# Optimization experiments

Hardware: AMD Instinct MI355X
Metric: run time of the kernel (lower is better)

The kernel has to match this reference:

```python
import jax, jax.numpy as jnp
import numpy as np

BN_EPS = 1e-5


def setup_inputs() -> dict:
    key = jax.random.key(0)
    ks = jax.random.split(key, 12)
    N, F, H, E, ED, G, EMB = 59392, 116, 256, 950272, 5, 8, 16
    return {
        "x": jax.random.normal(ks[0], (N, F), dtype=jnp.float32),
        "edge_index": jax.random.randint(ks[1], (2, E), 0, N, dtype=jnp.int64),
        "edge_attr": jax.random.normal(ks[2], (E, ED), dtype=jnp.float32),
        "group_ids": jax.random.randint(ks[3], (N,), 0, G, dtype=jnp.int64),
        "group_emb": jax.random.normal(ks[4], (G, EMB), dtype=jnp.float32),
        "W_in": jax.random.normal(ks[5], (F + EMB, H), dtype=jnp.float32) * 0.05,
        "b_in": jnp.zeros((H,), dtype=jnp.float32),
        "gamma": jnp.ones((H,), dtype=jnp.float32),
        "beta": jnp.zeros((H,), dtype=jnp.float32),
        "We": jax.random.normal(ks[6], (ED, H), dtype=jnp.float32) * 0.05,
        "be": jnp.zeros((H,), dtype=jnp.float32),
        "W1": jax.random.normal(ks[7], (H, H), dtype=jnp.float32) * 0.05,
        "b1": jnp.zeros((H,), dtype=jnp.float32),
        "W2": jax.random.normal(ks[8], (H, H), dtype=jnp.float32) * 0.05,
        "b2": jnp.zeros((H,), dtype=jnp.float32),
    }


def reference(x, edge_index, edge_attr, group_ids, group_emb, W_in, b_in,
              gamma, beta, We, be, W1, b1, W2, b2):
    N = x.shape[0]
    # group-embedding concat (dropout is identity in eval mode)
    h = jnp.concatenate([x, group_emb[group_ids]], axis=-1)      # [N, F+EMB]
    # dynamically-created Linear + ReLU
    h = jax.nn.relu(h @ W_in + b_in)                              # [N, H]
    # BatchNorm over nodes (training stats, biased var)
    mu = jnp.mean(h, axis=0)
    var = jnp.mean(jnp.square(h - mu), axis=0)
    h = (h - mu) * jax.lax.rsqrt(var + BN_EPS) * gamma + beta
    # GINEConv: msg = ReLU(x_j + lin(edge_attr)); sum-aggregate at target
    src, dst = edge_index[0], edge_index[1]
    msg = jax.nn.relu(h[src] + edge_attr @ We + be)               # [E, H]
    agg = jax.ops.segment_sum(msg, dst, num_segments=N)          # [N, H]
    z = h + agg                                                   # (1+eps)*h, eps=0
    out = jax.nn.relu(z @ W1 + b1) @ W2 + b2                      # 2-layer MLP
    out = jax.nn.relu(out)
    return (out, edge_attr)
```

## Files before the change

### kernel.cpp

```cpp
#include <hip/hip_runtime.h>
#include <hip/hip_bf16.h>
#include <cstdint>
#include <cstddef>

#define H 256
#define EMB 16
#define ED 5
#define BN_EPS 1e-5f

typedef __attribute__((ext_vector_type(8))) short short8;
typedef __attribute__((ext_vector_type(4))) float f32x4;
typedef _Float16 h2 __attribute__((ext_vector_type(2)));
typedef unsigned int u32x2 __attribute__((ext_vector_type(2)));

__device__ __forceinline__ unsigned short f2bf(float f) {
  unsigned int u = __float_as_uint(f);
  unsigned int r = (u + 0x7fffu + ((u >> 16) & 1u)) >> 16;
  return (unsigned short)r;
}
__device__ __forceinline__ unsigned int pk2bf(float a, float b) {
  return (unsigned int)f2bf(a) | ((unsigned int)f2bf(b) << 16);
}
__device__ __forceinline__ float bfhi(unsigned int u) {
  return __uint_as_float(u & 0xffff0000u);
}
__device__ __forceinline__ float bflo(unsigned int u) {
  return __uint_as_float(u << 16);
}
__device__ __forceinline__ h2 u2h2(unsigned int u) {
  union { unsigned int u; h2 h; } c;
  c.u = u;
  return c.h;
}
__device__ __forceinline__ unsigned int h22u(h2 h) {
  union { h2 h; unsigned int u; } c;
  c.h = h;
  return c.u;
}
__device__ __forceinline__ h2 mkh2(float a, float b) {
  h2 r;
  r.x = (_Float16)a;
  r.y = (_Float16)b;
  return r;
}

__global__ __launch_bounds__(256) void prep_kernel(
    const float* __restrict__ Win, const float* __restrict__ W1,
    const float* __restrict__ W2, const float* __restrict__ gemb,
    const float* __restrict__ b_in, unsigned short* __restrict__ Wtx,
    unsigned short* __restrict__ Wt1, unsigned short* __restrict__ Wt2,
    float* __restrict__ T, float* __restrict__ stats, int* __restrict__ deg,
    unsigned short* __restrict__ hbn, uint4* __restrict__ rec,
    int N, int F, int G, int E) {
  int idx = blockIdx.x * 256 + threadIdx.x;
  if (idx < 1024) stats[idx] = 0.f;
  if (idx < N) deg[idx] = 0;
  if (idx < 32)
    ((uint4*)(hbn + (size_t)N * H))[idx] =
        make_uint4(0xF400F400u, 0xF400F400u, 0xF400F400u, 0xF400F400u);
  if (idx == 0) rec[E] = make_uint4(((unsigned)N) << 9, 0u, 0u, 0u);
  if (idx < 256 * 128) {
    int n = idx >> 7, k = idx & 127;
    Wtx[idx] = f2bf((k < F) ? Win[(size_t)k * H + n] : 0.f);
  } else if (idx < 256 * 128 + 65536) {
    int i2 = idx - 256 * 128;
    int n = i2 >> 8, k = i2 & 255;
    Wt1[i2] = f2bf(W1[(size_t)k * H + n]);
  } else if (idx < 256 * 128 + 131072) {
    int i2 = idx - 256 * 128 - 65536;
    int n = i2 >> 8, k = i2 & 255;
    Wt2[i2] = f2bf(W2[(size_t)k * H + n]);
  } else if (idx < 256 * 128 + 131072 + G * 256) {
    int i2 = idx - 256 * 128 - 131072;
    int g = i2 >> 8, c = i2 & 255;
    float s = b_in[c];
    #pragma unroll
    for (int k = 0; k < EMB; ++k)
      s = fmaf(gemb[g * EMB + k], Win[(size_t)(F + k) * H + c], s);
    T[i2] = s;
  }
}

__global__ __launch_bounds__(256) void gemm_in_kernel(
    const float* __restrict__ x, const int* __restrict__ gid,
    const unsigned short* __restrict__ Wtx, const float* __restrict__ T,
    unsigned short* __restrict__ h0, float* __restrict__ stats, int F) {
  const int m0 = blockIdx.y * 128;
  const int n0 = blockIdx.x * 128;
  const int tid = threadIdx.x;
  const int lane = tid & 63;
  const int wave = tid >> 6;
  const int wm = (wave & 1) * 64;
  const int wn = (wave >> 1) * 64;
  const int l16 = lane & 15;
  const int quad = lane >> 4;
  __shared__ __align__(16) unsigned short As[128][40];
  __shared__ __align__(16) unsigned short Bs[128][40];
  __shared__ float cs[128], css[128];
  if (tid < 128) {
    cs[tid] = 0.f;
    css[tid] = 0.f;
  }
  f32x4 acc[4][4] = {};
  const int srow = tid >> 1;
  const int half = tid & 1;
  for (int k0 = 0; k0 < 128; k0 += 32) {
    __syncthreads();
    {
      const float* xp = x + (size_t)(m0 + srow) * F;
      float4 xv[4];
      #pragma unroll
      for (int f = 0; f < 4; ++f) {
        int c = k0 + half * 16 + f * 4;
        xv[f] = (c < F) ? *(const float4*)(xp + c)
                        : make_float4(0.f, 0.f, 0.f, 0.f);
      }
      uint4 p0, p1;
      p0.x = pk2bf(xv[0].x, xv[0].y); p0.y = pk2bf(xv[0].z, xv[0].w);
      p0.z = pk2bf(xv[1].x, xv[1].y); p0.w = pk2bf(xv[1].z, xv[1].w);
      p1.x = pk2bf(xv[2].x, xv[2].y); p1.y = pk2bf(xv[2].z, xv[2].w);
      p1.z = pk2bf(xv[3].x, xv[3].y); p1.w = pk2bf(xv[3].z, xv[3].w);
      *(uint4*)(&As[srow][half * 16]) = p0;
      *(uint4*)(&As[srow][half * 16 + 8]) = p1;
    }
    {
      const unsigned short* wp = Wtx + (size_t)(n0 + srow) * 128 + k0 + half * 16;
      *(uint4*)(&Bs[srow][half * 16]) = *(const uint4*)wp;
      *(uint4*)(&Bs[srow][half * 16 + 8]) = *(const uint4*)(wp + 8);
    }
    __syncthreads();
    short8 af[4], bf[4];
    #pragma unroll
    for (int i = 0; i < 4; ++i)
      af[i] = *(const short8*)(&As[wm + i * 16 + l16][quad * 8]);
    #pragma unroll
    for (int j = 0; j < 4; ++j)
      bf[j] = *(const short8*)(&Bs[wn + j * 16 + l16][quad * 8]);
    #pragma unroll
    for (int i = 0; i < 4; ++i)
      #pragma unroll
      for (int j = 0; j < 4; ++j)
        acc[i][j] = __builtin_amdgcn_mfma_f32_16x16x32_bf16(af[i], bf[j],
                                                            acc[i][j], 0, 0, 0);
  }
  int gi[4][4];
  #pragma unroll
  for (int i = 0; i < 4; ++i)
    #pragma unroll
    for (int r = 0; r < 4; ++r)
      gi[i][r] = gid[m0 + wm + i * 16 + quad * 4 + r];
  float ls[4] = {}, lss[4] = {};
  #pragma unroll
  for (int j = 0; j < 4; ++j) {
    const int col = n0 + wn + j * 16 + l16;
    #pragma unroll
    for (int i = 0; i < 4; ++i) {
      #pragma unroll
      for (int r = 0; r < 4; ++r) {
        const int row = m0 + wm + i * 16 + quad * 4 + r;
        float v = fmaxf(acc[i][j][r] + T[gi[i][r] * H + col], 0.f);
        h0[(size_t)row * H + col] = f2bf(v);
        ls[j] += v;
        lss[j] = fmaf(v, v, lss[j]);
      }
    }
  }
  #pragma unroll
  for (int j = 0; j < 4; ++j) {
    const int lc = wn + j * 16 + l16;
    atomicAdd(&cs[lc], ls[j]);
    atomicAdd(&css[lc], lss[j]);
  }
  __syncthreads();
  if (tid < 128) {
    atomicAdd(&stats[n0 + tid], cs[tid]);
    atomicAdd(&stats[H + n0 + tid], css[tid]);
  }
}

__global__ __launch_bounds__(256) void mlp_kernel(
    const unsigned short* __restrict__ z, const unsigned short* __restrict__ Wt1,
    const unsigned short* __restrict__ Wt2, const float* __restrict__ b1,
    const float* __restrict__ b2, float* __restrict__ out) {
  const int m0 = blockIdx.x * 64;
  const int tid = threadIdx.x;
  const int lane = tid & 63;
  const int wave = tid >> 6;
  const int wn = wave * 64;
  const int l16 = lane & 15;
  const int quad = lane >> 4;
  __shared__ __align__(16) unsigned short As[64][40];
  __shared__ __align__(16) unsigned short Bs[256][40];
  __shared__ __align__(16) unsigned short hidS[64][264];
  f32x4 acc[4][4] = {};
  const int ar = tid >> 2, ac = tid & 3;
  for (int k0 = 0; k0 < 256; k0 += 32) {
    __syncthreads();
    *(float4*)(&As[ar][ac * 8]) =
        *(const float4*)(z + (size_t)(m0 + ar) * H + k0 + ac * 8);
    #pragma unroll
    for (int t = 0; t < 4; ++t) {
      int r = ar + t * 64;
      *(float4*)(&Bs[r][ac * 8]) =
          *(const float4*)(Wt1 + (size_t)r * H + k0 + ac * 8);
    }
    __syncthreads();
    short8 af[4], bf[4];
    #pragma unroll
    for (int i = 0; i < 4; ++i)
      af[i] = *(const short8*)(&As[i * 16 + l16][quad * 8]);
    #pragma unroll
    for (int j = 0; j < 4; ++j)
      bf[j] = *(const short8*)(&Bs[wn + j * 16 + l16][quad * 8]);
    #pragma unroll
    for (int i = 0; i < 4; ++i)
      #pragma unroll
      for (int j = 0; j < 4; ++j)
        acc[i][j] = __builtin_amdgcn_mfma_f32_16x16x32_bf16(af[i], bf[j],
                                                            acc[i][j], 0, 0, 0);
  }
  #pragma unroll
  for (int j = 0; j < 4; ++j) {
    const int col = wn + j * 16 + l16;
    const float bj = b1[col];
    #pragma unroll
    for (int i = 0; i < 4; ++i)
      #pragma unroll
      for (int r = 0; r < 4; ++r) {
        const int row = i * 16 + quad * 4 + r;
        hidS[row][col] = f2bf(fmaxf(acc[i][j][r] + bj, 0.f));
      }
  }
  #pragma unroll
  for (int i = 0; i < 4; ++i)
    #pragma unroll
    for (int j = 0; j < 4; ++j)
      acc[i][j] = (f32x4){0.f, 0.f, 0.f, 0.f};
  for (int k0 = 0; k0 < 256; k0 += 32) {
    __syncthreads();
    #pragma unroll
    for (int t = 0; t < 4; ++t) {
      int r = ar + t * 64;
      *(float4*)(&Bs[r][ac * 8]) =
          *(const float4*)(Wt2 + (size_t)r * H + k0 + ac * 8);
    }
    __syncthreads();
    short8 af[4], bf[4];
    #pragma unroll
    for (int i = 0; i < 4; ++i)
      af[i] = *(const short8*)(&hidS[i * 16 + l16][k0 + quad * 8]);
    #pragma unroll
    for (int j = 0; j < 4; ++j)
      bf[j] = *(const short8*)(&Bs[wn + j * 16 + l16][quad * 8]);
    #pragma unroll
    for (int i = 0; i < 4; ++i)
      #pragma unroll
      for (int j = 0; j < 4; ++j)
        acc[i][j] = __builtin_amdgcn_mfma_f32_16x16x32_bf16(af[i], bf[j],
                                                            acc[i][j], 0, 0, 0);
  }
  #pragma unroll
  for (int j = 0; j < 4; ++j) {
    const int col = wn + j * 16 + l16;
    const float bj = b2[col];
    #pragma unroll
    for (int i = 0; i < 4; ++i)
      #pragma unroll
      for (int r = 0; r < 4; ++r) {
        const int row = m0 + i * 16 + quad * 4 + r;
        out[(size_t)row * H + col] = fmaxf(acc[i][j][r] + bj, 0.f);
      }
  }
}

__global__ __launch_bounds__(256) void hbn_kernel(
    const unsigned short* __restrict__ h0, const float* __restrict__ stats,
    const float* __restrict__ gamma, const float* __restrict__ beta,
    const float* __restrict__ be, unsigned short* __restrict__ hbn,
    float inv_n) {
  __shared__ float sa[H], sb[H];
  {
    const int j = threadIdx.x;
    const float mu = stats[j] * inv_n;
    const float var = stats[H + j] * inv_n - mu * mu;
    const float rs = 1.0f / sqrtf(var + BN_EPS);
    const float a = gamma[j] * rs;
    sa[j] = a;
    sb[j] = beta[j] - mu * a + be[j];
  }
  __syncthreads();
  const size_t i = (size_t)blockIdx.x * 256 + threadIdx.x;
  const int c = ((int)(i & 31)) * 8;
  const uint4 hv = ((const uint4*)h0)[i];
  float r[8] = {bflo(hv.x), bfhi(hv.x), bflo(hv.y), bfhi(hv.y),
                bflo(hv.z), bfhi(hv.z), bflo(hv.w), bfhi(hv.w)};
  float o[8];
  #pragma unroll
  for (int t = 0; t < 8; ++t)
    o[t] = fmaf(sa[c + t], r[t], sb[c + t]);
  uint4 ov;
  ov.x = h22u(mkh2(o[0], o[1]));
  ov.y = h22u(mkh2(o[2], o[3]));
  ov.z = h22u(mkh2(o[4], o[5]));
  ov.w = h22u(mkh2(o[6], o[7]));
  ((uint4*)hbn)[i] = ov;
}

__global__ __launch_bounds__(256) void csr_count_kernel(
    const int* __restrict__ ei, int* __restrict__ deg, int E) {
  int e = blockIdx.x * 256 + threadIdx.x;
  if (e < E) atomicAdd(&deg[ei[E + e]], 1);
}

__global__ __launch_bounds__(256) void scan_blocks_kernel(
    const int* __restrict__ deg, int* __restrict__ excl,
    int* __restrict__ bsums, int n) {
  const int tid = threadIdx.x;
  const int i = blockIdx.x * 256 + tid;
  const int lane = tid & 63, wid = tid >> 6;
  int v = (i < n) ? deg[i] : 0;
  int x = v;
  #pragma unroll
  for (int d = 1; d < 64; d <<= 1) {
    int y = __shfl_up(x, d, 64);
    if (lane >= d) x += y;
  }
  __shared__ int ws[4], wo[4];
  if (lane == 63) ws[wid] = x;
  __syncthreads();
  if (tid == 0) {
    int a = 0;
    #pragma unroll
    for (int w = 0; w < 4; ++w) { wo[w] = a; a += ws[w]; }
    bsums[blockIdx.x] = a;
  }
  __syncthreads();
  if (i < n) excl[i] = x - v + wo[wid];
}

__global__ __launch_bounds__(256) void scan_finish_kernel(
    int* __restrict__ row_start, int* __restrict__ cursor,
    const int* __restrict__ bsums, int n, int E, int NB) {
  const int tid = threadIdx.x;
  const int b = blockIdx.x;
  int v = (tid < b && tid < NB) ? bsums[tid] : 0;
  int s = v;
  #pragma unroll
  for (int d = 32; d > 0; d >>= 1) s += __shfl_down(s, d, 64);
  __shared__ int ws[4];
  if ((tid & 63) == 0) ws[tid >> 6] = s;
  __syncthreads();
  const int S = ws[0] + ws[1] + ws[2] + ws[3];
  const int i = b * 256 + tid;
  if (i < n) {
    int r = row_start[i] + S;
    row_start[i] = r;
    cursor[i] = r;
  }
  if (b == 0 && tid == 0) row_start[n] = E;
}

__global__ __launch_bounds__(256) void csr_scatter_kernel(
    const int* __restrict__ ei, const float* __restrict__ ea,
    int* __restrict__ cursor, uint4* __restrict__ rec,
    float* __restrict__ ea_out, int E) {
  int e = blockIdx.x * 256 + threadIdx.x;
  if (e >= E) return;
  int s = ei[e];
  int d = ei[E + e];
  int p = atomicAdd(&cursor[d], 1);
  const float* eap = ea + (size_t)e * ED;
  const float e0 = eap[0], e1 = eap[1], e2 = eap[2], e3 = eap[3], e4 = eap[4];
  uint4 r;
  r.x = ((unsigned)s) << 9;
  r.y = h22u(mkh2(e0, e1));
  r.z = h22u(mkh2(e2, e3));
  r.w = h22u(mkh2(e4, 0.f));
  rec[p] = r;
  float* op = ea_out + (size_t)e * ED;
  op[0] = e0; op[1] = e1; op[2] = e2; op[3] = e3; op[4] = e4;
}

__device__ __forceinline__ void edge_accum(
    const uint4 rr, const u32x2 hv, const h2 wA[5], const h2 wB[5],
    float& ax, float& ay, float& az, float& aw) {
  h2 m01 = u2h2(hv.x);
  h2 m23 = u2h2(hv.y);
  const h2 e01 = u2h2(rr.y), e23 = u2h2(rr.z), e44 = u2h2(rr.w);
  h2 t;
  t.x = e01.x; t.y = e01.x;  m01 += t * wA[0]; m23 += t * wB[0];
  t.x = e01.y; t.y = e01.y;  m01 += t * wA[1]; m23 += t * wB[1];
  t.x = e23.x; t.y = e23.x;  m01 += t * wA[2]; m23 += t * wB[2];
  t.x = e23.y; t.y = e23.y;  m01 += t * wA[3]; m23 += t * wB[3];
  t.x = e44.x; t.y = e44.x;  m01 += t * wA[4]; m23 += t * wB[4];
  const h2 z2 = {(_Float16)0.f, (_Float16)0.f};
  m01 = __builtin_elementwise_max(m01, z2);
  m23 = __builtin_elementwise_max(m23, z2);
  ax += (float)m01.x;
  ay += (float)m01.y;
  az += (float)m23.x;
  aw += (float)m23.y;
}

__global__ __launch_bounds__(256) void aggregate_kernel(
    const unsigned short* __restrict__ hbn, const uint4* __restrict__ rec,
    const float* __restrict__ We, const float* __restrict__ be,
    const int* __restrict__ row_start, unsigned short* __restrict__ z,
    int N, int E) {
  const int lane = threadIdx.x & 63;
  int n = blockIdx.x * 4 + (threadIdx.x >> 6);
  if (n >= N) return;
  n = __builtin_amdgcn_readfirstlane(n);
  const int c = lane * 4;
  const int c2 = c << 1;
  const float4 be4 = *(const float4*)(be + c);
  h2 wA[5], wB[5];
  #pragma unroll
  for (int k = 0; k < 5; ++k) {
    wA[k] = mkh2(We[k * H + c], We[k * H + c + 1]);
    wB[k] = mkh2(We[k * H + c + 2], We[k * H + c + 3]);
  }
  float ax = 0.f, ay = 0.f, az = 0.f, aw = 0.f;
  const int s0 = __builtin_amdgcn_readfirstlane(row_start[n]);
  const int s1 = __builtin_amdgcn_readfirstlane(row_start[n + 1]);
  const int cnt = s1 - s0;
  const int sentIdx = E - s0;
  const uint4* rp = rec + s0;
  const char* hb = (const char*)hbn;
  const int nb = (cnt + 15) >> 4;
  for (int b = 0; b < nb; ++b) {
    const int base = b << 4;
    uint4 rr[16];
    #pragma unroll
    for (int u = 0; u < 16; ++u) {
      int idx = base + u;
      idx = (idx < cnt) ? idx : sentIdx;
      rr[u] = rp[idx];
    }
    u32x2 hh[16];
    #pragma unroll
    for (int u = 0; u < 16; ++u) {
      const unsigned short* bp = (const unsigned short*)(hb + rr[u].x);
      asm volatile("global_load_dwordx2 %0, %1, %2"
                   : "=&v"(hh[u])
                   : "v"(c2), "s"(bp)
                   : "memory");
    }
    asm volatile("s_waitcnt vmcnt(0)" ::: "memory");
    __builtin_amdgcn_sched_barrier(0);
    #pragma unroll
    for (int u = 0; u < 16; ++u)
      edge_accum(rr[u], hh[u], wA, wB, ax, ay, az, aw);
  }
  const uint2 hs = *(const uint2*)(hbn + (size_t)n * H + c);
  const h2 hsA = u2h2(hs.x), hsB = u2h2(hs.y);
  float zx = (float)hsA.x - be4.x + ax;
  float zy = (float)hsA.y - be4.y + ay;
  float zz = (float)hsB.x - be4.z + az;
  float zw = (float)hsB.y - be4.w + aw;
  uint2 o;
  o.x = pk2bf(zx, zy);
  o.y = pk2bf(zz, zw);
  *(uint2*)(z + (size_t)n * H + c) = o;
}

extern "C" void kernel_launch(void* const* d_in, const int* in_sizes, int n_in,
                              void* d_out, int out_size, void* d_ws, size_t ws_size,
                              hipStream_t stream) {
  const float* x     = (const float*)d_in[0];
  const int*   ei    = (const int*)d_in[1];
  const float* ea    = (const float*)d_in[2];
  const int*   gid   = (const int*)d_in[3];
  const float* gemb  = (const float*)d_in[4];
  const float* W_in  = (const float*)d_in[5];
  const float* b_in  = (const float*)d_in[6];
  const float* gamma = (const float*)d_in[7];
  const float* beta  = (const float*)d_in[8];
  const float* We    = (const float*)d_in[9];
  const float* be    = (const float*)d_in[10];
  const float* W1    = (const float*)d_in[11];
  const float* b1    = (const float*)d_in[12];
  const float* W2    = (const float*)d_in[13];
  const float* b2    = (const float*)d_in[14];
  float* out = (float*)d_out;

  const int N = in_sizes[3];
  const int E = in_sizes[1] / 2;
  const int F = in_sizes[0] / N;
  const int G = in_sizes[4] / EMB;
  const int NB = (N + 255) / 256;

  char* p = (char*)d_ws;
  auto take = [&](size_t bytes) {
    char* r = p;
    p += (bytes + 255) & ~(size_t)255;
    return r;
  };
  float* stats          = (float*)take(1024 * sizeof(float));
  int* deg              = (int*)take((size_t)N * 4);
  int* row_start        = (int*)take((size_t)(N + 1) * 4);
  int* cursor           = (int*)take((size_t)N * 4);
  int* bsums            = (int*)take((size_t)NB * 4);
  uint4* rec            = (uint4*)take((size_t)(E + 1) * 16);
  unsigned short* Wtx   = (unsigned short*)take((size_t)256 * 128 * 2);
  unsigned short* Wt1   = (unsigned short*)take((size_t)H * H * 2);
  unsigned short* Wt2   = (unsigned short*)take((size_t)H * H * 2);
  float* T              = (float*)take((size_t)G * H * 4);
  unsigned short* h0    = (unsigned short*)take((size_t)N * H * 2);
  unsigned short* hbn   = (unsigned short*)take((size_t)(N + 1) * H * 2);
  unsigned short* z     = (unsigned short*)take((size_t)N * H * 2);

  {
    int total = 256 * 128 + 131072 + G * 256;
    int nb = (total + 255) / 256;
    if (nb < (N + 255) / 256) nb = (N + 255) / 256;
    prep_kernel<<<nb, 256, 0, stream>>>(W_in, W1, W2, gemb, b_in, Wtx, Wt1,
                                        Wt2, T, stats, deg, hbn, rec, N, F, G, E);
  }

  csr_count_kernel<<<(E + 255) / 256, 256, 0, stream>>>(ei, deg, E);
  scan_blocks_kernel<<<NB, 256, 0, stream>>>(deg, row_start, bsums, N);
  scan_finish_kernel<<<NB, 256, 0, stream>>>(row_start, cursor, bsums, N, E, NB);
  csr_scatter_kernel<<<(E + 255) / 256, 256, 0, stream>>>(
      ei, ea, cursor, rec, out + (size_t)N * H, E);

  dim3 ggrid(H / 128, N / 128);
  gemm_in_kernel<<<ggrid, 256, 0, stream>>>(x, gid, Wtx, T, h0, stats, F);

  hbn_kernel<<<((size_t)N * H / 8) / 256, 256, 0, stream>>>(
      h0, stats, gamma, beta, be, hbn, 1.0f / (float)N);

  aggregate_kernel<<<(N + 3) / 4, 256, 0, stream>>>(hbn, rec, We, be,
                                                    row_start, z, N, E);

  mlp_kernel<<<N / 64, 256, 0, stream>>>(z, Wt1, Wt2, b1, b2, out);
}
```

Baseline: 396.7 us.

## Split aggregation across feature slices and edge-parallel quarter-waves

The aggregate kernel now launches eight times more blocks. Each block handles one 32-column slice of the hidden dimension. Within a wave, four 16-lane groups each take every fourth edge and gather only 4 bytes of h per lane, then combine their partial sums with cross-lane shuffles. The old 16-deep batched gather with inline asm is replaced by a one-ahead prefetch of edge records using nontemporal loads. The goal is more parallelism and latency hiding for the irregular gather. In exchange, each edge record is read eight times, once per slice, and each gather is narrower.

```diff
diff --git a/kernel.cpp b/kernel.cpp
--- a/kernel.cpp
+++ b/kernel.cpp
@@ -11,7 +11,7 @@
 typedef __attribute__((ext_vector_type(8))) short short8;
 typedef __attribute__((ext_vector_type(4))) float f32x4;
 typedef _Float16 h2 __attribute__((ext_vector_type(2)));
-typedef unsigned int u32x2 __attribute__((ext_vector_type(2)));
+typedef unsigned int u32x4 __attribute__((ext_vector_type(4)));
 
 __device__ __forceinline__ unsigned short f2bf(float f) {
   unsigned int u = __float_as_uint(f);
@@ -381,87 +381,70 @@
   op[0] = e0; op[1] = e1; op[2] = e2; op[3] = e3; op[4] = e4;
 }
 
-__device__ __forceinline__ void edge_accum(
-    const uint4 rr, const u32x2 hv, const h2 wA[5], const h2 wB[5],
-    float& ax, float& ay, float& az, float& aw) {
-  h2 m01 = u2h2(hv.x);
-  h2 m23 = u2h2(hv.y);
-  const h2 e01 = u2h2(rr.y), e23 = u2h2(rr.z), e44 = u2h2(rr.w);
-  h2 t;
-  t.x = e01.x; t.y = e01.x;  m01 += t * wA[0]; m23 += t * wB[0];
-  t.x = e01.y; t.y = e01.y;  m01 += t * wA[1]; m23 += t * wB[1];
-  t.x = e23.x; t.y = e23.x;  m01 += t * wA[2]; m23 += t * wB[2];
-  t.x = e23.y; t.y = e23.y;  m01 += t * wA[3]; m23 += t * wB[3];
-  t.x = e44.x; t.y = e44.x;  m01 += t * wA[4]; m23 += t * wB[4];
-  const h2 z2 = {(_Float16)0.f, (_Float16)0.f};
-  m01 = __builtin_elementwise_max(m01, z2);
-  m23 = __builtin_elementwise_max(m23, z2);
-  ax += (float)m01.x;
-  ay += (float)m01.y;
-  az += (float)m23.x;
-  aw += (float)m23.y;
-}
-
 __global__ __launch_bounds__(256) void aggregate_kernel(
     const unsigned short* __restrict__ hbn, const uint4* __restrict__ rec,
     const float* __restrict__ We, const float* __restrict__ be,
     const int* __restrict__ row_start, unsigned short* __restrict__ z,
     int N, int E) {
-  const int lane = threadIdx.x & 63;
-  int n = blockIdx.x * 4 + (threadIdx.x >> 6);
+  const int tid = threadIdx.x;
+  const int lane = tid & 63;
+  const int wave = tid >> 6;
+  const int slice = blockIdx.x & 7;
+  int n = (blockIdx.x >> 3) * 4 + wave;
   if (n >= N) return;
   n = __builtin_amdgcn_readfirstlane(n);
-  const int c = lane * 4;
-  const int c2 = c << 1;
-  const float4 be4 = *(const float4*)(be + c);
-  h2 wA[5], wB[5];
+  const int l16 = lane & 15;
+  const int q = lane >> 4;
+  const int c = slice * 32 + l16 * 2;
+  const int hoff = slice * 64 + l16 * 4;
+  const float2 be2 = *(const float2*)(be + c);
+  h2 w[5];
   #pragma unroll
   for (int k = 0; k < 5; ++k) {
-    wA[k] = mkh2(We[k * H + c], We[k * H + c + 1]);
-    wB[k] = mkh2(We[k * H + c + 2], We[k * H + c + 3]);
-  }
-  float ax = 0.f, ay = 0.f, az = 0.f, aw = 0.f;
+    float2 wk = *(const float2*)(We + k * H + c);
+    w[k] = mkh2(wk.x, wk.y);
+  }
+  float ax = 0.f, ay = 0.f;
   const int s0 = __builtin_amdgcn_readfirstlane(row_start[n]);
   const int s1 = __builtin_amdgcn_readfirstlane(row_start[n + 1]);
   const int cnt = s1 - s0;
   const int sentIdx = E - s0;
-  const uint4* rp = rec + s0;
+  const u32x4* rp = (const u32x4*)(rec + s0);
   const char* hb = (const char*)hbn;
-  const int nb = (cnt + 15) >> 4;
-  for (int b = 0; b < nb; ++b) {
-    const int base = b << 4;
-    uint4 rr[16];
-    #pragma unroll
-    for (int u = 0; u < 16; ++u) {
-      int idx = base + u;
-      idx = (idx < cnt) ? idx : sentIdx;
-      rr[u] = rp[idx];
+  const h2 z2 = {(_Float16)0.f, (_Float16)0.f};
+  if (cnt > 0) {
+    int idx0 = (q < cnt) ? q : sentIdx;
+    u32x4 rr = __builtin_nontemporal_load(rp + idx0);
+    for (int i = 0; i < cnt; i += 4) {
+      int inx = i + 4 + q;
+      inx = (inx < cnt) ? inx : sentIdx;
+      u32x4 rn = __builtin_nontemporal_load(rp + inx);
+      const unsigned hv = *(const unsigned*)(hb + (rr.x + hoff));
+      h2 m = u2h2(hv);
+      const h2 e01 = u2h2(rr.y), e23 = u2h2(rr.z), e44 = u2h2(rr.w);
+      m += __builtin_shufflevector(e01, e01, 0, 0) * w[0];
+      m += __builtin_shufflevector(e01, e01, 1, 1) * w[1];
+      m += __builtin_shufflevector(e23, e23, 0, 0) * w[2];
+      m += __builtin_shufflevector(e23, e23, 1, 1) * w[3];
+      m += __builtin_shufflevector(e44, e44, 0, 0) * w[4];
+      m = __builtin_elementwise_max(m, z2);
+      ax += (float)m.x;
+      ay += (float)m.y;
+      rr = rn;
     }
-    u32x2 hh[16];
-    #pragma unroll
-    for (int u = 0; u < 16; ++u) {
-      const unsigned short* bp = (const unsigned short*)(hb + rr[u].x);
-      asm volatile("global_load_dwordx2 %0, %1, %2"
-                   : "=&v"(hh[u])
-                   : "v"(c2), "s"(bp)
-                   : "memory");
-    }
-    asm volatile("s_waitcnt vmcnt(0)" ::: "memory");
-    __builtin_amdgcn_sched_barrier(0);
-    #pragma unroll
-    for (int u = 0; u < 16; ++u)
-      edge_accum(rr[u], hh[u], wA, wB, ax, ay, az, aw);
-  }
-  const uint2 hs = *(const uint2*)(hbn + (size_t)n * H + c);
-  const h2 hsA = u2h2(hs.x), hsB = u2h2(hs.y);
-  float zx = (float)hsA.x - be4.x + ax;
-  float zy = (float)hsA.y - be4.y + ay;
-  float zz = (float)hsB.x - be4.z + az;
-  float zw = (float)hsB.y - be4.w + aw;
-  uint2 o;
-  o.x = pk2bf(zx, zy);
-  o.y = pk2bf(zz, zw);
-  *(uint2*)(z + (size_t)n * H + c) = o;
+  }
+  ax += __shfl_xor(ax, 16, 64);
+  ay += __shfl_xor(ay, 16, 64);
+  ax += __shfl_xor(ax, 32, 64);
+  ay += __shfl_xor(ay, 32, 64);
+  if (q == 0) {
+    const unsigned hs = *(const unsigned*)(hb + ((size_t)n << 9) + hoff);
+    const h2 hsA = u2h2(hs);
+    const float zx = (float)hsA.x - be2.x + ax;
+    const float zy = (float)hsA.y - be2.y + ay;
+    __builtin_nontemporal_store(pk2bf(zx, zy),
+                                (unsigned*)(z + (size_t)n * H + c));
+  }
 }
 
 extern "C" void kernel_launch(void* const* d_in, const int* in_sizes, int n_in,
@@ -530,8 +513,11 @@
   hbn_kernel<<<((size_t)N * H / 8) / 256, 256, 0, stream>>>(
       h0, stats, gamma, beta, be, hbn, 1.0f / (float)N);
 
-  aggregate_kernel<<<(N + 3) / 4, 256, 0, stream>>>(hbn, rec, We, be,
-                                                    row_start, z, N, E);
+  {
+    int nblk = ((N + 3) / 4) * 8;
+    aggregate_kernel<<<nblk, 256, 0, stream>>>(hbn, rec, We, be,
+                                               row_start, z, N, E);
+  }
 
   mlp_kernel<<<N / 64, 256, 0, stream>>>(z, Wt1, Wt2, b1, b2, out);
 }
```

New measurement: 705.7 us. 77.9% more time.
